# Optimization experiments

Hardware: AMD Instinct MI355X
Metric: run time of the kernel (lower is better)

The kernel has to match this reference:

```python
import jax, jax.numpy as jnp
import numpy as np

# RNN-T joint network: broadcast encoder (B,T,D) and decoder (B,U,D) states,
# concat on feature dim -> (B,T,U,2D), then Linear(2D -> C, bias=False).
# Mathematically identical efficient form: split W = [W_enc | W_dec] along its
# input dim and compute two small GEMMs + broadcast add, avoiding the (B,T,U,2D)
# intermediate. cat(e,d) @ W^T == e @ W_enc^T + d @ W_dec^T.

B, T, U, D, C = 4, 256, 64, 512, 1024


def setup_inputs() -> dict:
    key = jax.random.key(0)
    k1, k2, k3 = jax.random.split(key, 3)
    encoder_outputs = jax.random.normal(k1, (B, T, D), dtype=jnp.float32)
    decoder_outputs = jax.random.normal(k2, (B, U, D), dtype=jnp.float32)
    # fc weight: (num_classes, 2*encoder_dim), torch Linear layout
    W = jax.random.normal(k3, (C, 2 * D), dtype=jnp.float32) * (1.0 / np.sqrt(2 * D))
    return {"encoder_outputs": encoder_outputs, "decoder_outputs": decoder_outputs, "W": W}


def reference(encoder_outputs, decoder_outputs, W):
    d = encoder_outputs.shape[-1]
    W_enc, W_dec = W[:, :d], W[:, d:]
    # (B,T,C) and (B,U,C), then broadcast add -> (B,T,U,C)
    enc_proj = jnp.einsum("btd,cd->btc", encoder_outputs, W_enc)
    dec_proj = jnp.einsum("bud,cd->buc", decoder_outputs, W_dec)
    return enc_proj[:, :, None, :] + dec_proj[:, None, :, :]
```

## Files before the change

### kernel.cpp

```cpp
#include <hip/hip_runtime.h>
#include <hip/hip_bf16.h>


typedef float v4f   __attribute__((ext_vector_type(4)));
typedef float f32x4 __attribute__((ext_vector_type(4)));
typedef __attribute__((ext_vector_type(8))) short short8;

__device__ inline short bf16_of(float f) {
    __hip_bfloat16 h = __float2bfloat16(f);
    return *reinterpret_cast<short*>(&h);
}

__global__ __launch_bounds__(256) void cvt_frag(
    const float* __restrict__ enc, const float* __restrict__ dec,
    const float* __restrict__ W,
    ushort* __restrict__ Xe_f, ushort* __restrict__ Xd_f,
    ushort* __restrict__ We_f, ushort* __restrict__ Wd_f)
{
    const int tid  = threadIdx.x;
    const int lane = tid & 63;
    const int l16  = lane & 15;
    const int kq   = lane >> 4;
    const int gid  = blockIdx.x * 4 + (tid >> 6);

    const float* src; ushort* dst; int g, rowStride, colOfs;
    if (gid < 1024)      { src = enc; dst = Xe_f; g = gid;        rowStride = 512;  colOfs = 0;   }
    else if (gid < 1280) { src = dec; dst = Xd_f; g = gid - 1024; rowStride = 512;  colOfs = 0;   }
    else if (gid < 2304) { src = W;   dst = We_f; g = gid - 1280; rowStride = 1024; colOfs = 0;   }
    else                 { src = W;   dst = Wd_f; g = gid - 2304; rowStride = 1024; colOfs = 512; }

    const int rb  = g >> 4;
    const int kbi = g & 15;
    const float* p = src + (size_t)(rb * 16 + l16) * rowStride + colOfs + kbi * 32 + kq * 8;
    float4 lo = *(const float4*)p;
    float4 hi = *(const float4*)(p + 4);
    short8 o;
    o[0] = bf16_of(lo.x); o[1] = bf16_of(lo.y); o[2] = bf16_of(lo.z); o[3] = bf16_of(lo.w);
    o[4] = bf16_of(hi.x); o[5] = bf16_of(hi.y); o[6] = bf16_of(hi.z); o[7] = bf16_of(hi.w);
    *(short8*)&dst[(size_t)g * 512 + lane * 8] = o;
}

__global__ __launch_bounds__(256) void dec_gemm_bf16(
    const ushort* __restrict__ Xd_f,
    const ushort* __restrict__ Wd_f,
    float* __restrict__ Pd)
{
    const int tid  = threadIdx.x;
    const int wave = tid >> 6;
    const int lane = tid & 63;
    const int l16  = lane & 15;
    const int kq   = lane >> 4;

    const int kz = wave >> 1;
    const int wn = (wave & 1) * 32;
    const int mb = blockIdx.y;
    const int cBase = blockIdx.x * 64;
    const int cb0 = blockIdx.x * 4 + (wave & 1) * 2;

    const short8* xa  = (const short8*)Xd_f + (size_t)(mb  * 16 + kz * 8) * 64 + lane;
    const short8* wb0 = (const short8*)Wd_f + (size_t)(cb0       * 16 + kz * 8) * 64 + lane;
    const short8* wb1 = (const short8*)Wd_f + (size_t)((cb0 + 1) * 16 + kz * 8) * 64 + lane;

    f32x4 acc0 = {0.f,0.f,0.f,0.f}, acc1 = {0.f,0.f,0.f,0.f};
#pragma unroll
    for (int s = 0; s < 8; ++s) {
        short8 a  = xa [(size_t)s * 64];
        short8 b0 = wb0[(size_t)s * 64];
        short8 b1 = wb1[(size_t)s * 64];
        acc0 = __builtin_amdgcn_mfma_f32_16x16x32_bf16(a, b0, acc0, 0, 0, 0);
        acc1 = __builtin_amdgcn_mfma_f32_16x16x32_bf16(a, b1, acc1, 0, 0, 0);
    }

    __shared__ float Ps[16][65];
    if (kz == 1) {
#pragma unroll
        for (int r = 0; r < 4; ++r) {
            Ps[kq * 4 + r][wn + l16]      = acc0[r];
            Ps[kq * 4 + r][wn + 16 + l16] = acc1[r];
        }
    }
    __syncthreads();
    if (kz == 0) {
        float* p0 = Pd + (size_t)(mb * 16) * 1024 + cBase + wn;
#pragma unroll
        for (int r = 0; r < 4; ++r) {
            const int row = kq * 4 + r;
            p0[(size_t)row * 1024 + l16]      = acc0[r] + Ps[row][wn + l16];
            p0[(size_t)row * 1024 + 16 + l16] = acc1[r] + Ps[row][wn + 16 + l16];
        }
    }
}

__global__ __launch_bounds__(256) void fused_enc_stream(
    const ushort* __restrict__ Xe_f,
    const ushort* __restrict__ We_f,
    const float* __restrict__ Pd,
    float* __restrict__ out)
{
    const int tid  = threadIdx.x;
    const int kz   = tid >> 6;
    const int lane = tid & 63;
    const int l16  = lane & 15;
    const int kq   = lane >> 4;

    const int btBase = blockIdx.y * 16;
    const int cBase  = blockIdx.x * 64;
    const int b      = blockIdx.y >> 4;

    __shared__ float encS[4][16][68];
    __shared__ float decS[64][64];

    float4 v0, v1, v2, v3;
    {
        int s0 = tid;
        v0 = *(const float4*)&Pd[(size_t)(b * 64 + ((s0          ) >> 4)) * 1024 + cBase + ((s0          ) & 15) * 4];
        v1 = *(const float4*)&Pd[(size_t)(b * 64 + ((s0 + 256    ) >> 4)) * 1024 + cBase + ((s0 + 256    ) & 15) * 4];
        v2 = *(const float4*)&Pd[(size_t)(b * 64 + ((s0 + 512    ) >> 4)) * 1024 + cBase + ((s0 + 512    ) & 15) * 4];
        v3 = *(const float4*)&Pd[(size_t)(b * 64 + ((s0 + 768    ) >> 4)) * 1024 + cBase + ((s0 + 768    ) & 15) * 4];
    }

    {
        const short8* xa = (const short8*)Xe_f + (size_t)(blockIdx.y * 16 + kz * 4) * 64 + lane;
        const short8* wb = (const short8*)We_f + (size_t)(kz * 4) * 64 + lane;
        f32x4 acc[4] = {{0.f,0.f,0.f,0.f},{0.f,0.f,0.f,0.f},{0.f,0.f,0.f,0.f},{0.f,0.f,0.f,0.f}};
#pragma unroll
        for (int s = 0; s < 4; ++s) {
            short8 a = xa[(size_t)s * 64];
#pragma unroll
            for (int j = 0; j < 4; ++j) {
                short8 bf = wb[((size_t)(blockIdx.x * 4 + j) * 16 + s) * 64];
                acc[j] = __builtin_amdgcn_mfma_f32_16x16x32_bf16(a, bf, acc[j], 0, 0, 0);
            }
        }
#pragma unroll
        for (int j = 0; j < 4; ++j)
#pragma unroll
            for (int r = 0; r < 4; ++r)
                encS[kz][kq * 4 + r][j * 16 + l16] = acc[j][r];
    }

    {
        int s0 = tid;
        *(float4*)&decS[(s0          ) >> 4][((s0          ) & 15) * 4] = v0;
        *(float4*)&decS[(s0 + 256    ) >> 4][((s0 + 256    ) & 15) * 4] = v1;
        *(float4*)&decS[(s0 + 512    ) >> 4][((s0 + 512    ) & 15) * 4] = v2;
        *(float4*)&decS[(s0 + 768    ) >> 4][((s0 + 768    ) & 15) * 4] = v3;
    }

    __syncthreads();

    const int row = tid >> 4;
    const int c4  = (tid & 15) * 4;

    const float4 e0 = *(const float4*)&encS[0][row][c4];
    const float4 e1 = *(const float4*)&encS[1][row][c4];
    const float4 e2 = *(const float4*)&encS[2][row][c4];
    const float4 e3 = *(const float4*)&encS[3][row][c4];
    const v4f e = {e0.x + e1.x + e2.x + e3.x,
                   e0.y + e1.y + e2.y + e3.y,
                   e0.z + e1.z + e2.z + e3.z,
                   e0.w + e1.w + e2.w + e3.w};

    float* po = out + (size_t)(btBase + row) * 64 * 1024 + cBase + c4;

#pragma unroll 8
    for (int u = 0; u < 64; ++u) {
        float4 d = *(const float4*)&decS[u][c4];
        v4f r = {e.x + d.x, e.y + d.y, e.z + d.z, e.w + d.w};
        __builtin_nontemporal_store(r, (v4f*)&po[(size_t)u * 1024]);
    }
}

extern "C" void kernel_launch(void* const* d_in, const int* in_sizes, int n_in,
                              void* d_out, int out_size, void* d_ws, size_t ws_size,
                              hipStream_t stream) {
    const float* enc = (const float*)d_in[0];
    const float* dec = (const float*)d_in[1];
    const float* W   = (const float*)d_in[2];
    float* out = (float*)d_out;

    char* ws = (char*)d_ws;
    float*  Pd   = (float*)(ws);
    ushort* Xe_f = (ushort*)(ws + (1u << 20));
    ushort* Xd_f = (ushort*)(ws + (2u << 20));
    ushort* We_f = (ushort*)(ws + (2u << 20) + (1u << 18));
    ushort* Wd_f = (ushort*)(ws + (3u << 20) + (1u << 18));

    cvt_frag<<<dim3(832), 256, 0, stream>>>(enc, dec, W, Xe_f, Xd_f, We_f, Wd_f);
    dec_gemm_bf16<<<dim3(16, 16), 256, 0, stream>>>(Xd_f, Wd_f, Pd);
    fused_enc_stream<<<dim3(16, 64), 256, 0, stream>>>(Xe_f, We_f, Pd, out);
}
```

Measured before the change: 65.07 us.

## Widen encoder tile to 256 columns and stream decoder projection directly

The fused kernel now gives each block 256 output columns instead of 64. Each wave computes a full-K MMA for its own 64 columns, so the split-K reduction through shared memory goes away. The decoder projection is read straight from global memory inside the store loop and reused across 4 rows, instead of being staged into shared memory. The grid shrinks from 1024 to 256 blocks, which lowers parallelism for a store-bound kernel and lengthens each wave's serial MFMA chain.

```diff
diff --git a/kernel.cpp b/kernel.cpp
--- a/kernel.cpp
+++ b/kernel.cpp
@@ -98,37 +98,29 @@
     float* __restrict__ out)
 {
     const int tid  = threadIdx.x;
-    const int kz   = tid >> 6;
+    const int w    = tid >> 6;
     const int lane = tid & 63;
     const int l16  = lane & 15;
     const int kq   = lane >> 4;
 
     const int btBase = blockIdx.y * 16;
-    const int cBase  = blockIdx.x * 64;
+    const int cBase  = blockIdx.x * 256;
     const int b      = blockIdx.y >> 4;
 
-    __shared__ float encS[4][16][68];
-    __shared__ float decS[64][64];
-
-    float4 v0, v1, v2, v3;
-    {
-        int s0 = tid;
-        v0 = *(const float4*)&Pd[(size_t)(b * 64 + ((s0          ) >> 4)) * 1024 + cBase + ((s0          ) & 15) * 4];
-        v1 = *(const float4*)&Pd[(size_t)(b * 64 + ((s0 + 256    ) >> 4)) * 1024 + cBase + ((s0 + 256    ) & 15) * 4];
-        v2 = *(const float4*)&Pd[(size_t)(b * 64 + ((s0 + 512    ) >> 4)) * 1024 + cBase + ((s0 + 512    ) & 15) * 4];
-        v3 = *(const float4*)&Pd[(size_t)(b * 64 + ((s0 + 768    ) >> 4)) * 1024 + cBase + ((s0 + 768    ) & 15) * 4];
-    }
+    __shared__ float encS[16][264];
 
     {
-        const short8* xa = (const short8*)Xe_f + (size_t)(blockIdx.y * 16 + kz * 4) * 64 + lane;
-        const short8* wb = (const short8*)We_f + (size_t)(kz * 4) * 64 + lane;
-        f32x4 acc[4] = {{0.f,0.f,0.f,0.f},{0.f,0.f,0.f,0.f},{0.f,0.f,0.f,0.f},{0.f,0.f,0.f,0.f}};
+        const short8* xa    = (const short8*)Xe_f + (size_t)(blockIdx.y * 16) * 64 + lane;
+        const short8* wbase = (const short8*)We_f + lane;
+        f32x4 acc[4] = {{0.f,0.f,0.f,0.f},{0.f,0.f,0.f,0.f},
+                        {0.f,0.f,0.f,0.f},{0.f,0.f,0.f,0.f}};
 #pragma unroll
-        for (int s = 0; s < 4; ++s) {
+        for (int s = 0; s < 16; ++s) {
             short8 a = xa[(size_t)s * 64];
 #pragma unroll
             for (int j = 0; j < 4; ++j) {
-                short8 bf = wb[((size_t)(blockIdx.x * 4 + j) * 16 + s) * 64];
+                const int cb = blockIdx.x * 16 + w * 4 + j;
+                short8 bf = wbase[(size_t)(cb * 16 + s) * 64];
                 acc[j] = __builtin_amdgcn_mfma_f32_16x16x32_bf16(a, bf, acc[j], 0, 0, 0);
             }
         }
@@ -136,38 +128,27 @@
         for (int j = 0; j < 4; ++j)
 #pragma unroll
             for (int r = 0; r < 4; ++r)
-                encS[kz][kq * 4 + r][j * 16 + l16] = acc[j][r];
-    }
-
-    {
-        int s0 = tid;
-        *(float4*)&decS[(s0          ) >> 4][((s0          ) & 15) * 4] = v0;
-        *(float4*)&decS[(s0 + 256    ) >> 4][((s0 + 256    ) & 15) * 4] = v1;
-        *(float4*)&decS[(s0 + 512    ) >> 4][((s0 + 512    ) & 15) * 4] = v2;
-        *(float4*)&decS[(s0 + 768    ) >> 4][((s0 + 768    ) & 15) * 4] = v3;
+                encS[kq * 4 + r][(w * 4 + j) * 16 + l16] = acc[j][r];
     }
 
     __syncthreads();
 
-    const int row = tid >> 4;
-    const int c4  = (tid & 15) * 4;
+    float4 e[4];
+#pragma unroll
+    for (int i = 0; i < 4; ++i)
+        e[i] = *(const float4*)&encS[w * 4 + i][lane * 4];
 
-    const float4 e0 = *(const float4*)&encS[0][row][c4];
-    const float4 e1 = *(const float4*)&encS[1][row][c4];
-    const float4 e2 = *(const float4*)&encS[2][row][c4];
-    const float4 e3 = *(const float4*)&encS[3][row][c4];
-    const v4f e = {e0.x + e1.x + e2.x + e3.x,
-                   e0.y + e1.y + e2.y + e3.y,
-                   e0.z + e1.z + e2.z + e3.z,
-                   e0.w + e1.w + e2.w + e3.w};
-
-    float* po = out + (size_t)(btBase + row) * 64 * 1024 + cBase + c4;
+    const float* pd = Pd + (size_t)(b * 64) * 1024 + cBase + lane * 4;
+    float*       po = out + (size_t)(btBase + w * 4) * 64 * 1024 + cBase + lane * 4;
 
 #pragma unroll 8
     for (int u = 0; u < 64; ++u) {
-        float4 d = *(const float4*)&decS[u][c4];
-        v4f r = {e.x + d.x, e.y + d.y, e.z + d.z, e.w + d.w};
-        __builtin_nontemporal_store(r, (v4f*)&po[(size_t)u * 1024]);
+        float4 d = *(const float4*)&pd[(size_t)u * 1024];
+#pragma unroll
+        for (int i = 0; i < 4; ++i) {
+            v4f r = {e[i].x + d.x, e[i].y + d.y, e[i].z + d.z, e[i].w + d.w};
+            __builtin_nontemporal_store(r, (v4f*)&po[((size_t)i * 64 + u) * 1024]);
+        }
     }
 }
 
@@ -188,5 +169,5 @@
 
     cvt_frag<<<dim3(832), 256, 0, stream>>>(enc, dec, W, Xe_f, Xd_f, We_f, Wd_f);
     dec_gemm_bf16<<<dim3(16, 16), 256, 0, stream>>>(Xd_f, Wd_f, Pd);
-    fused_enc_stream<<<dim3(16, 64), 256, 0, stream>>>(Xe_f, We_f, Pd, out);
+    fused_enc_stream<<<dim3(4, 64), 256, 0, stream>>>(Xe_f, We_f, Pd, out);
 }
```

Result: slower. 74.89 us (+15.1%).
